# Kernel tuning notes

Hardware: AMD Instinct MI355X
Metric: run time of the kernel (lower is better)

The kernel has to match this reference:

```python
import jax, jax.numpy as jnp
import numpy as np

NUM_TOKENS = 32000
DIM = 1024
DEPTH = 4
HEADS = 16
DIM_HEAD = 64
FF_MULT = 4
DH_FF = int(DIM * FF_MULT * 2 / 3)  # 2730
B, N = 2, 2048
ROPE_THETA = 10000.0


def setup_inputs() -> dict:
    key = jax.random.key(0)
    ks = jax.random.split(key, 8)
    s = 0.02
    return {
        "tokens": jax.random.randint(ks[0], (B, N), 0, NUM_TOKENS),
        "token_emb": jax.random.normal(ks[1], (NUM_TOKENS, DIM)) * s,
        "attn_norm_w": jnp.ones((DEPTH, DIM)),
        "wqkv": jax.random.normal(ks[2], (DEPTH, DIM, 3 * HEADS * DIM_HEAD)) * s,
        "wo": jax.random.normal(ks[3], (DEPTH, HEADS * DIM_HEAD, DIM)) * s,
        "ff_norm_w": jnp.ones((DEPTH, DIM)),
        "ff_w1": jax.random.normal(ks[4], (DEPTH, DIM, 2 * DH_FF)) * s,
        "ff_b1": jnp.zeros((DEPTH, 2 * DH_FF)),
        "ff_w2": jax.random.normal(ks[5], (DEPTH, DH_FF, DIM)) * s,
        "ff_b2": jnp.zeros((DEPTH, DIM)),
        "final_norm_w": jnp.ones((DIM,)),
        "logits_w": jax.random.normal(ks[6], (DIM, NUM_TOKENS)) * s,
        "logits_b": jnp.zeros((NUM_TOKENS,)),
    }


def rmsnorm(x, w):
    eps = jnp.finfo(x.dtype).eps  # torch RMSNorm default eps
    var = jnp.mean(jnp.square(x), axis=-1, keepdims=True)
    return x * jax.lax.rsqrt(var + eps) * w


def rotate_half(x):
    x1, x2 = jnp.split(x, 2, axis=-1)
    return jnp.concatenate((-x2, x1), axis=-1)


def apply_rope(pos, t):
    return t * jnp.cos(pos) + rotate_half(t) * jnp.sin(pos)


def reference(tokens, token_emb, attn_norm_w, wqkv, wo, ff_norm_w,
              ff_w1, ff_b1, ff_w2, ff_b2, final_norm_w, logits_w, logits_b):
    b, n = tokens.shape
    x = token_emb[tokens]  # [b, n, dim]

    # rotary embedding table [n, dim_head]
    inv_freq = ROPE_THETA ** (-(jnp.arange(0, DIM_HEAD, 2, dtype=jnp.float32) / DIM_HEAD))
    freqs = jnp.arange(n, dtype=jnp.float32)[:, None] * inv_freq[None, :]
    pos = jnp.concatenate((freqs, freqs), axis=-1)

    scale = DIM_HEAD ** -0.5
    causal = jnp.triu(jnp.ones((n, n), dtype=bool), 1)

    for l in range(DEPTH):
        # --- attention ---
        h = rmsnorm(x, attn_norm_w[l])
        qkv = jnp.einsum('bnd,de->bne', h, wqkv[l])
        qkv = qkv.reshape(b, n, 3, HEADS, DIM_HEAD)
        qkv = jnp.transpose(qkv, (2, 0, 3, 1, 4))  # [3, b, h, n, d]
        q, k, v = qkv[0], qkv[1], qkv[2]
        q = apply_rope(pos, q)
        k = apply_rope(pos, k)
        q = q * scale
        sim = jnp.einsum('bhid,bhjd->bhij', q, k)
        sim = jnp.where(causal, -jnp.finfo(sim.dtype).max, sim)
        attn = jax.nn.softmax(sim, axis=-1)
        out = jnp.einsum('bhij,bhjd->bhid', attn, v)
        out = jnp.transpose(out, (0, 2, 1, 3)).reshape(b, n, HEADS * DIM_HEAD)
        x = jnp.einsum('bne,ed->bnd', out, wo[l]) + x

        # --- GEGLU feedforward ---
        h = rmsnorm(x, ff_norm_w[l])
        u = jnp.einsum('bnd,de->bne', h, ff_w1[l]) + ff_b1[l]
        u1, gate = jnp.split(u, 2, axis=-1)
        g = jax.nn.gelu(gate, approximate=False) * u1
        x = jnp.einsum('bne,ed->bnd', g, ff_w2[l]) + ff_b2[l] + x

    embed = rmsnorm(x, final_norm_w)
    logits = jnp.einsum('bnd,dv->bnv', embed, logits_w) + logits_b
    return logits
```

## Files before the change

kernel.cpp:

```cpp
#include <hip/hip_runtime.h>
#include <math.h>
#include <stdint.h>


using short8v = __attribute__((ext_vector_type(8))) short;
using f32x4   = __attribute__((ext_vector_type(4))) float;

__device__ __forceinline__ float b2f(short s) {
    union { unsigned u; float f; } v; v.u = ((unsigned)(unsigned short)s) << 16; return v.f;
}
__device__ __forceinline__ short f2b(float f) {
    union { float f; unsigned u; } v; v.f = f;
    unsigned r = v.u + 0x7FFFu + ((v.u >> 16) & 1u);
    return (short)(r >> 16);
}

__device__ __forceinline__ void mfma_n(f32x4& d, short8v a, short8v b) {
    asm("v_mfma_f32_16x16x32_bf16 %0, %1, %2, %0" : "+v"(d) : "v"(a), "v"(b));
}
__device__ __forceinline__ void mfma_f(f32x4& d, short8v a, short8v b) {
    asm("s_nop 1\n\tv_mfma_f32_16x16x32_bf16 %0, %1, %2, %0" : "+v"(d) : "v"(a), "v"(b));
}
#define MFMA_FENCE() do { __builtin_amdgcn_sched_barrier(0); \
    asm volatile("s_nop 7\n\ts_nop 7"); \
    __builtin_amdgcn_sched_barrier(0); } while (0)

__device__ __forceinline__ void gload16(const void* g, void* l) {
    __builtin_amdgcn_global_load_lds(
        (const __attribute__((address_space(1))) unsigned int*)(uintptr_t)g,
        (__attribute__((address_space(3))) unsigned int*)(uintptr_t)l,
        16, 0, 0);
}

#define BARX() do { asm volatile("" ::: "memory"); \
    __builtin_amdgcn_s_barrier(); asm volatile("" ::: "memory"); } while (0)
#define VMN(n) asm volatile("s_waitcnt vmcnt(" #n ")" ::: "memory")
#define LGKM0() do { asm volatile("s_waitcnt lgkmcnt(0)" ::: "memory"); \
    __builtin_amdgcn_sched_barrier(0); } while (0)

__global__ void rope_table_k(float* __restrict__ ct, float* __restrict__ st) {
    int i = blockIdx.x * 256 + threadIdx.x;
    int n = i >> 5, j = i & 31;
    float freq = expf(-(float)j * (9.210340371976184f / 32.f));
    float a = (float)n * freq;
    ct[i] = cosf(a);
    st[i] = sinf(a);
}

__global__ void embed_k(const int* __restrict__ tok, const float* __restrict__ emb,
                        float* __restrict__ x) {
    int row = blockIdx.x;
    int tk = tok[row];
    const float4* src = (const float4*)(emb + (size_t)tk * 1024);
    float4* dst = (float4*)(x + (size_t)row * 1024);
    dst[threadIdx.x] = src[threadIdx.x];
}

__global__ void wconv_k(const float* __restrict__ W, short* __restrict__ T,
                        int K, int N, int Kpad,
                        size_t w_lstride, size_t t_lstride) {
    W += blockIdx.z * w_lstride;
    T += blockIdx.z * t_lstride;
    int n0 = blockIdx.x * 32, k0 = blockIdx.y * 32;
    __shared__ float tile[32][33];
    int t = threadIdx.x;
    int kk = t >> 3, ns = (t & 7) * 4;
    float4 v = make_float4(0.f, 0.f, 0.f, 0.f);
    int gk = k0 + kk;
    if (gk < K) {
        if (n0 + ns + 3 < N) {
            v = *(const float4*)(W + (size_t)gk * N + n0 + ns);
        } else {
            float tmp[4] = {0.f, 0.f, 0.f, 0.f};
            #pragma unroll
            for (int j = 0; j < 4; ++j)
                if (n0 + ns + j < N) tmp[j] = W[(size_t)gk * N + n0 + ns + j];
            v = make_float4(tmp[0], tmp[1], tmp[2], tmp[3]);
        }
    }
    tile[kk][ns + 0] = v.x; tile[kk][ns + 1] = v.y;
    tile[kk][ns + 2] = v.z; tile[kk][ns + 3] = v.w;
    __syncthreads();
    int nn = t >> 3, ks = (t & 7) * 4;
    short o[4];
    #pragma unroll
    for (int j = 0; j < 4; ++j) o[j] = f2b(tile[ks + j][nn]);
    *(int2*)(T + (size_t)(n0 + nn) * Kpad + k0 + ks) = *(int2*)o;
}

__global__ void rmsnorm_k(const float* __restrict__ x, const float* __restrict__ wt,
                          short* __restrict__ out) {
    int row = blockIdx.x;
    int t = threadIdx.x;
    const float* xr = x + (size_t)row * 1024;
    float4 v = ((const float4*)xr)[t];
    float ss = v.x * v.x + v.y * v.y + v.z * v.z + v.w * v.w;
    #pragma unroll
    for (int off = 32; off > 0; off >>= 1) ss += __shfl_down(ss, off, 64);
    __shared__ float red[4];
    if ((t & 63) == 0) red[t >> 6] = ss;
    __syncthreads();
    float tot = red[0] + red[1] + red[2] + red[3];
    float inv = rsqrtf(tot * (1.f / 1024.f) + 1.1920929e-7f);
    float4 wv = ((const float4*)wt)[t];
    int2 pk;
    pk.x = (int)(unsigned short)f2b(v.x * inv * wv.x) |
           ((int)(unsigned short)f2b(v.y * inv * wv.y) << 16);
    pk.y = (int)(unsigned short)f2b(v.z * inv * wv.z) |
           ((int)(unsigned short)f2b(v.w * inv * wv.w) << 16);
    *(int2*)(out + (size_t)row * 1024 + t * 4) = pk;
}

__global__ void vt_k(const short* __restrict__ qkv, short* __restrict__ vt) {
    int id = blockIdx.x * 256 + threadIdx.x;
    int dt = id & 7, nt = (id >> 3) & 255, bh = id >> 11;
    int b = bh >> 4, h = bh & 15;
    short s[8][8];
    #pragma unroll
    for (int r = 0; r < 8; ++r)
        *(int4*)s[r] = *(const int4*)(qkv + (size_t)(b * 2048 + nt * 8 + r) * 3072
                                      + 2048 + h * 64 + dt * 8);
    #pragma unroll
    for (int cc = 0; cc < 8; ++cc) {
        short o4[8];
        #pragma unroll
        for (int r = 0; r < 8; ++r) o4[r] = s[r][cc];
        *(int4*)(vt + (size_t)(bh * 64 + dt * 8 + cc) * 2048 + nt * 8) = *(int4*)o4;
    }
}

__global__ void geglu_k(const short* __restrict__ u, short* __restrict__ gbuf) {
    int r = blockIdx.x;
    int c = blockIdx.y * 256 + threadIdx.x;
    if (c >= 2752) return;
    float v = 0.f;
    if (c < 2730) {
        float u1 = b2f(u[(size_t)r * 5460 + c]);
        float gt = b2f(u[(size_t)r * 5460 + 2730 + c]);
        v = 0.5f * gt * (1.f + erff(gt * 0.7071067811865475f)) * u1;
    }
    gbuf[(size_t)r * 2752 + c] = f2b(v);
}

template <bool BIAS, bool RES, bool OUTBF16>
__global__ __launch_bounds__(256, 2) void gemm2(
    const short* __restrict__ A, const short* __restrict__ Bt,
    const float* __restrict__ bias, const float* __restrict__ res,
    void* __restrict__ outp, int N, int lda, int ldb, int ksteps) {
    __shared__ __align__(16) short As[128 * 32];
    __shared__ __align__(16) short Bs[128 * 32];
    const int t = threadIdx.x;
    const int lane = t & 63;
    const int w = t >> 6, wm = w >> 1, wn = w & 1;
    const int c = lane & 15, g = lane >> 4;

    const int nwg = (int)gridDim.x;
    const int cpx = nwg >> 3;
    const int wg = ((int)blockIdx.x & 7) * cpx + ((int)blockIdx.x >> 3);
    const int m0 = (wg & 31) << 7;
    const int n0 = (wg >> 5) << 7;

    const int srow = w * 32 + (lane >> 2);
    const int sseg = (lane & 3) * 8;
    const short* ga0 = A  + (size_t)(m0 + srow) * lda + sseg;
    const short* ga1 = A  + (size_t)(m0 + srow + 16) * lda + sseg;
    const short* gb0 = Bt + (size_t)(n0 + srow) * ldb + sseg;
    const short* gb1 = Bt + (size_t)(n0 + srow + 16) * ldb + sseg;
    short* la0 = &As[(w * 2 + 0) * 512];
    short* la1 = &As[(w * 2 + 1) * 512];
    short* lb0 = &Bs[(w * 2 + 0) * 512];
    short* lb1 = &Bs[(w * 2 + 1) * 512];

    f32x4 acc[4][4] = {};

    for (int kt = 0; kt < ksteps; ++kt) {
        const int k0 = kt << 5;
        __syncthreads();
        gload16(ga0 + k0, la0);
        gload16(ga1 + k0, la1);
        gload16(gb0 + k0, lb0);
        gload16(gb1 + k0, lb1);
        __syncthreads();
        short8v af[4], bf[4];
        #pragma unroll
        for (int mi = 0; mi < 4; ++mi)
            af[mi] = *(const short8v*)&As[(wm * 64 + mi * 16 + c) * 32 + g * 8];
        #pragma unroll
        for (int ni = 0; ni < 4; ++ni)
            bf[ni] = *(const short8v*)&Bs[(wn * 64 + ni * 16 + c) * 32 + g * 8];
        #pragma unroll
        for (int mi = 0; mi < 4; ++mi)
            #pragma unroll
            for (int ni = 0; ni < 4; ++ni)
                mfma_n(acc[mi][ni], af[mi], bf[ni]);
    }
    MFMA_FENCE();
    #pragma unroll
    for (int mi = 0; mi < 4; ++mi) {
        #pragma unroll
        for (int ni = 0; ni < 4; ++ni) {
            int col = n0 + wn * 64 + ni * 16 + c;
            if (col < N) {
                float bv = BIAS ? bias[col] : 0.f;
                #pragma unroll
                for (int i = 0; i < 4; ++i) {
                    int row = m0 + wm * 64 + mi * 16 + g * 4 + i;
                    size_t off = (size_t)row * N + col;
                    float v = acc[mi][ni][i] + bv;
                    if (RES) v += res[off];
                    if (OUTBF16) ((short*)outp)[off] = f2b(v);
                    else         ((float*)outp)[off] = v;
                }
            }
        }
    }
}

template <bool BIAS, bool RES, bool OUTBF16, bool ROPE>
__global__ __launch_bounds__(512, 1) void gemm3(
    const short* __restrict__ A, const short* __restrict__ Bt,
    const float* __restrict__ bias, const float* __restrict__ res,
    void* __restrict__ outp, int N, int lda, int ldb, int nrowsB, int KT,
    const float* __restrict__ ct, const float* __restrict__ st) {
    __shared__ __align__(16) short L[49152];
    const int t = threadIdx.x;
    const int lane = t & 63;
    const int w = t >> 6;
    const int wm = w >> 2, wn = w & 3;
    const int c = lane & 15, g = lane >> 4;

    const int nwg = (int)gridDim.x, cpx = nwg >> 3;
    const int wg = ((int)blockIdx.x & 7) * cpx + ((int)blockIdx.x >> 3);
    const int m0 = (wg & 31) << 7;
    const int n0 = (wg >> 5) << 8;

    const int rS = t >> 3, sS = t & 7;
    const int sSw = (sS ^ (rS & 7)) << 3;
    size_t aoffh[2], broff[2][2];
    #pragma unroll
    for (int h = 0; h < 2; ++h)
        aoffh[h] = (size_t)(m0 + h * 64 + rS) * lda + sSw;
    #pragma unroll
    for (int h = 0; h < 2; ++h)
        #pragma unroll
        for (int i = 0; i < 2; ++i) {
            int brow = n0 + h * 128 + rS + i * 64;
            if (brow > nrowsB - 1) brow = nrowsB - 1;
            broff[h][i] = (size_t)brow * ldb + sSw;
        }
    short* ldsA[2][2];
    short* ldsB[2][2];
    #pragma unroll
    for (int p = 0; p < 2; ++p)
        #pragma unroll
        for (int h = 0; h < 2; ++h) {
            ldsA[p][h] = &L[(p * 2 + h) * 4096 + w * 512];
            ldsB[p][h] = &L[16384 + (p * 2 + h) * 8192 + w * 512];
        }

    const int cb0 = ((g * 8) ^ ((c & 7) * 8));
    const int vbA0 = wm * 4096 + c * 64 + cb0;
    const int vbA1 = vbA0 ^ 32;
    const int vbB0 = 16384 + (wn >> 1) * 8192 + (wn & 1) * 4096 + c * 64 + cb0;
    const int vbB1 = vbB0 ^ 32;

    #define STA3(p, h, kt) gload16(A + aoffh[h] + (kt) * 64, ldsA[p][h])
    #define STB3(p, h, kt) do { \
        gload16(Bt + broff[h][0] + (kt) * 64, ldsB[p][h]); \
        gload16(Bt + broff[h][1] + (kt) * 64, ldsB[p][h] + 4096); } while (0)
    #define LDA3(p, mi, ks) (*(const short8v*)&L[(p) * 8192 + (mi) * 1024 + ((ks) ? vbA1 : vbA0)])
    #define LDB3(p, ni, ks) (*(const short8v*)&L[(p) * 16384 + (ni) * 1024 + ((ks) ? vbB1 : vbB0)])
    #define MFMA8(MLO, NLO, BV) do { \
        _Pragma("unroll") for (int ks_ = 0; ks_ < 2; ++ks_) \
        _Pragma("unroll") for (int mi_ = 0; mi_ < 2; ++mi_) \
        _Pragma("unroll") for (int ni_ = 0; ni_ < 2; ++ni_) \
            mfma_n(acc[(MLO) + mi_][(NLO) + ni_], av[(MLO) + mi_][ks_], BV[(NLO) + ni_][ks_]); \
        } while (0)

    f32x4 acc[4][4] = {};
    short8v av[4][2], bc[4][2], bn[4][2];

    STB3(0, 1, 0); STB3(0, 0, 0); STA3(0, 0, 0); STA3(0, 1, 0);
    STB3(1, 1, 1); STB3(1, 0, 1); STA3(1, 0, 1); STA3(1, 1, 1);
    VMN(6);
    BARX();
    #pragma unroll
    for (int ni = 0; ni < 4; ++ni)
        #pragma unroll
        for (int ks = 0; ks < 2; ++ks)
            bc[ni][ks] = LDB3(0, ni, ks);
    LGKM0();
    BARX();
    asm volatile("s_nop 7\n\ts_nop 7");

    for (int KB = 0; KB < KT; KB += 2) {
        const bool st1 = (KB + 2 < KT);
        const bool st2 = (KB + 3 < KT);
        #pragma unroll
        for (int mi = 0; mi < 2; ++mi)
            #pragma unroll
            for (int ks = 0; ks < 2; ++ks) av[mi][ks] = LDA3(0, mi, ks);
        if (st1) STB3(0, 1, KB + 2);
        BARX();
        __builtin_amdgcn_s_setprio(1); MFMA8(0, 0, bc); __builtin_amdgcn_s_setprio(0);
        BARX();
        #pragma unroll
        for (int mi = 2; mi < 4; ++mi)
            #pragma unroll
            for (int ks = 0; ks < 2; ++ks) av[mi][ks] = LDA3(0, mi, ks);
        if (st1) { STB3(0, 0, KB + 2); VMN(6); } else { VMN(2); }
        BARX();
        __builtin_amdgcn_s_setprio(1); MFMA8(2, 0, bc); __builtin_amdgcn_s_setprio(0);
        BARX();
        #pragma unroll
        for (int ni = 0; ni < 2; ++ni)
            #pragma unroll
            for (int ks = 0; ks < 2; ++ks) bn[ni][ks] = LDB3(1, ni, ks);
        if (st1) STA3(0, 0, KB + 2);
        BARX();
        __builtin_amdgcn_s_setprio(1); MFMA8(0, 2, bc); __builtin_amdgcn_s_setprio(0);
        BARX();
        #pragma unroll
        for (int ni = 2; ni < 4; ++ni)
            #pragma unroll
            for (int ks = 0; ks < 2; ++ks) bn[ni][ks] = LDB3(1, ni, ks);
        if (st1) { STA3(0, 1, KB + 2); VMN(6); } else { VMN(0); }
        BARX();
        __builtin_amdgcn_s_setprio(1); MFMA8(2, 2, bc); __builtin_amdgcn_s_setprio(0);
        BARX();
        #pragma unroll
        for (int mi = 0; mi < 2; ++mi)
            #pragma unroll
            for (int ks = 0; ks < 2; ++ks) av[mi][ks] = LDA3(1, mi, ks);
        if (st2) STB3(1, 1, KB + 3);
        BARX();
        __builtin_amdgcn_s_setprio(1); MFMA8(0, 0, bn); __builtin_amdgcn_s_setprio(0);
        BARX();
        #pragma unroll
        for (int mi = 2; mi < 4; ++mi)
            #pragma unroll
            for (int ks = 0; ks < 2; ++ks) av[mi][ks] = LDA3(1, mi, ks);
        if (st2) STB3(1, 0, KB + 3);
        if (st1) VMN(6);
        BARX();
        __builtin_amdgcn_s_setprio(1); MFMA8(2, 0, bn); __builtin_amdgcn_s_setprio(0);
        BARX();
        if (st1) {
            #pragma unroll
            for (int ni = 0; ni < 2; ++ni)
                #pragma unroll
                for (int ks = 0; ks < 2; ++ks) bc[ni][ks] = LDB3(0, ni, ks);
        }
        if (st2) STA3(1, 0, KB + 3);
        BARX();
        __builtin_amdgcn_s_setprio(1); MFMA8(0, 2, bn); __builtin_amdgcn_s_setprio(0);
        BARX();
        if (st1) {
            #pragma unroll
            for (int ni = 2; ni < 4; ++ni)
                #pragma unroll
                for (int ks = 0; ks < 2; ++ks) bc[ni][ks] = LDB3(0, ni, ks);
        }
        if (st2) STA3(1, 1, KB + 3);
        if (st1) VMN(6);
        BARX();
        __builtin_amdgcn_s_setprio(1); MFMA8(2, 2, bn); __builtin_amdgcn_s_setprio(0);
        BARX();
    }

    MFMA_FENCE();

    if (ROPE) {
        const int colbase = n0 + wn * 64;
        const int sec = colbase >> 10;
        if (sec < 2) {
            const float sc = (sec == 0) ? 0.125f : 1.0f;
            #pragma unroll
            for (int mi = 0; mi < 4; ++mi)
                #pragma unroll
                for (int ni = 0; ni < 2; ++ni) {
                    const int col = colbase + ni * 16 + c;
                    const int jj = ni * 16 + c;
                    #pragma unroll
                    for (int i = 0; i < 4; ++i) {
                        int row = m0 + wm * 64 + mi * 16 + g * 4 + i;
                        int n = row & 2047;
                        float cv = ct[n * 32 + jj], sv = st[n * 32 + jj];
                        float a = acc[mi][ni][i], b = acc[mi][ni + 2][i];
                        ((short*)outp)[(size_t)row * N + col]      = f2b((a * cv - b * sv) * sc);
                        ((short*)outp)[(size_t)row * N + col + 32] = f2b((b * cv + a * sv) * sc);
                    }
                }
        } else {
            #pragma unroll
            for (int mi = 0; mi < 4; ++mi)
                #pragma unroll
                for (int ni = 0; ni < 4; ++ni) {
                    int col = colbase + ni * 16 + c;
                    #pragma unroll
                    for (int i = 0; i < 4; ++i) {
                        int row = m0 + wm * 64 + mi * 16 + g * 4 + i;
                        ((short*)outp)[(size_t)row * N + col] = f2b(acc[mi][ni][i]);
                    }
                }
        }
        return;
    }

    #pragma unroll
    for (int mi = 0; mi < 4; ++mi) {
        #pragma unroll
        for (int ni = 0; ni < 4; ++ni) {
            int col = n0 + wn * 64 + ni * 16 + c;
            if (col < N) {
                float bv = BIAS ? bias[col] : 0.f;
                #pragma unroll
                for (int i = 0; i < 4; ++i) {
                    int row = m0 + wm * 64 + mi * 16 + g * 4 + i;
                    size_t off = (size_t)row * N + col;
                    float v = acc[mi][ni][i] + bv;
                    if (RES) v += res[off];
                    if (OUTBF16) ((short*)outp)[off] = f2b(v);
                    else         ((float*)outp)[off] = v;
                }
            }
        }
    }
    #undef STA3
    #undef STB3
    #undef LDA3
    #undef LDB3
    #undef MFMA8
}

template <bool BIAS, bool RES, bool OUTBF16>
__global__ __launch_bounds__(512, 2) void gemm4(
    const short* __restrict__ A, const short* __restrict__ Bt,
    const float* __restrict__ bias, const float* __restrict__ res,
    void* __restrict__ outp, int N, int lda, int ldb, int nrowsB, int KT) {
    __shared__ __align__(16) short L[65536];
    const int t = threadIdx.x;
    const int lane = t & 63;
    const int w = t >> 6;
    const int wm = w >> 2, wn = w & 3;
    const int c = lane & 15, g = lane >> 4;

    const int nwg = (int)gridDim.x, cpx = nwg >> 3;
    const int wg = ((int)blockIdx.x & 7) * cpx + ((int)blockIdx.x >> 3);
    const int m0 = (wg & 15) << 8;
    const int n0 = (wg >> 4) << 8;

    const int sub0 = t & 63;
    const int seg0 = sub0 >> 4, r0 = sub0 & 15;
    const int slab0 = t >> 6, slab1 = slab0 + 8;
    const size_t aoff0 = (size_t)(m0 + slab0 * 16 + r0) * lda + seg0 * 8;
    const size_t aoff1 = (size_t)(m0 + slab1 * 16 + r0) * lda + seg0 * 8;
    int br0 = n0 + slab0 * 16 + r0; if (br0 > nrowsB - 1) br0 = nrowsB - 1;
    int br1 = n0 + slab1 * 16 + r0; if (br1 > nrowsB - 1) br1 = nrowsB - 1;
    const size_t boff0 = (size_t)br0 * ldb + seg0 * 8;
    const size_t boff1 = (size_t)br1 * ldb + seg0 * 8;

    char* Lb = (char*)L;
    const int rb = g * 256 + c * 16;

    #define STA4(p, kh, kt) do { \
        gload16(A + aoff0 + (kt) * 64 + (kh) * 32, Lb + ((p)*2+(kh))*16384 + w*1024); \
        gload16(A + aoff1 + (kt) * 64 + (kh) * 32, Lb + ((p)*2+(kh))*16384 + 8192 + w*1024); } while (0)
    #define STB4(p, kh, kt) do { \
        gload16(Bt + boff0 + (kt) * 64 + (kh) * 32, Lb + 65536 + ((p)*2+(kh))*16384 + w*1024); \
        gload16(Bt + boff1 + (kt) * 64 + (kh) * 32, Lb + 65536 + ((p)*2+(kh))*16384 + 8192 + w*1024); } while (0)
    #define LDA4(p, ks, mi) (*(const short8v*)(Lb + ((p)*2+(ks))*16384 + (wm*8+(mi))*1024 + rb))
    #define LDB4(p, ks, ni) (*(const short8v*)(Lb + 65536 + ((p)*2+(ks))*16384 + (wn*4+(ni))*1024 + rb))
    #define MFMAQ(MB) do { \
        _Pragma("unroll") for (int mi_ = 0; mi_ < 4; ++mi_) \
        _Pragma("unroll") for (int ni_ = 0; ni_ < 4; ++ni_) \
            mfma_n(acc[(MB) + mi_][ni_], av[mi_], bv[ni_]); } while (0)

    f32x4 acc[8][4] = {};
    short8v av[4], bv[4];

    STA4(0, 0, 0); STB4(0, 0, 0); STA4(0, 1, 0); STB4(0, 1, 0);
    VMN(4);
    BARX();
    asm volatile("s_nop 7\n\ts_nop 7");

    #define TILE4(p, pn, tc, stg2) do { \
        _Pragma("unroll") for (int mi = 0; mi < 4; ++mi) av[mi] = LDA4(p, 0, mi); \
        _Pragma("unroll") for (int ni = 0; ni < 4; ++ni) bv[ni] = LDB4(p, 0, ni); \
        if (stg2) STA4(pn, 0, (tc) + 1); \
        BARX(); \
        __builtin_amdgcn_s_setprio(1); MFMAQ(0); __builtin_amdgcn_s_setprio(0); \
        BARX(); \
        _Pragma("unroll") for (int mi = 0; mi < 4; ++mi) av[mi] = LDA4(p, 0, mi + 4); \
        if (stg2) { STB4(pn, 0, (tc) + 1); VMN(4); } else { VMN(0); } \
        BARX(); \
        __builtin_amdgcn_s_setprio(1); MFMAQ(4); __builtin_amdgcn_s_setprio(0); \
        BARX(); \
        _Pragma("unroll") for (int mi = 0; mi < 4; ++mi) av[mi] = LDA4(p, 1, mi); \
        _Pragma("unroll") for (int ni = 0; ni < 4; ++ni) bv[ni] = LDB4(p, 1, ni); \
        if (stg2) STA4(pn, 1, (tc) + 1); \
        BARX(); \
        __builtin_amdgcn_s_setprio(1); MFMAQ(0); __builtin_amdgcn_s_setprio(0); \
        BARX(); \
        _Pragma("unroll") for (int mi = 0; mi < 4; ++mi) av[mi] = LDA4(p, 1, mi + 4); \
        if (stg2) { STB4(pn, 1, (tc) + 1); VMN(4); } \
        BARX(); \
        __builtin_amdgcn_s_setprio(1); MFMAQ(4); __builtin_amdgcn_s_setprio(0); \
        BARX(); \
    } while (0)

    for (int kt = 0; kt < KT; kt += 2) {
        TILE4(0, 1, kt, true);
        TILE4(1, 0, kt + 1, (kt + 2 < KT));
    }
    #undef TILE4

    MFMA_FENCE();
    #pragma unroll
    for (int mi = 0; mi < 8; ++mi) {
        #pragma unroll
        for (int ni = 0; ni < 4; ++ni) {
            int col = n0 + wn * 64 + ni * 16 + c;
            if (col < N) {
                float bvv = BIAS ? bias[col] : 0.f;
                #pragma unroll
                for (int i = 0; i < 4; ++i) {
                    int row = m0 + wm * 128 + mi * 16 + g * 4 + i;
                    size_t off = (size_t)row * N + col;
                    float v = acc[mi][ni][i] + bvv;
                    if (RES) v += res[off];
                    if (OUTBF16) ((short*)outp)[off] = f2b(v);
                    else         ((float*)outp)[off] = v;
                }
            }
        }
    }
    #undef STA4
    #undef STB4
    #undef LDA4
    #undef LDB4
    #undef MFMAQ
}

__global__ __launch_bounds__(256, 2) void attn_fwd(
    const short* __restrict__ qkv, const short* __restrict__ vt,
    short* __restrict__ o) {
    const int qt = blockIdx.x, bh = blockIdx.y;
    const int b = bh >> 4, h = bh & 15;
    const int t = threadIdx.x, lane = t & 63, w = t >> 6;
    const int c = lane & 15, g = lane >> 4;
    __shared__ __align__(16) short Ks[128 * 72];
    __shared__ __align__(16) short Vs[64 * 136];
    __shared__ __align__(16) short Ps[128 * 136];

    #pragma unroll
    for (int i = 0; i < 4; ++i) {
        int idx = t + i * 256, r = idx >> 3, seg = idx & 7;
        *(int4*)&Ps[r * 136 + seg * 8] =
            *(const int4*)(qkv + (size_t)(b * 2048 + qt * 128 + r) * 3072 + h * 64 + seg * 8);
    }
    __syncthreads();
    short8v qf[2][2];
    #pragma unroll
    for (int mi = 0; mi < 2; ++mi)
        #pragma unroll
        for (int kk = 0; kk < 2; ++kk)
            qf[mi][kk] = *(const short8v*)&Ps[(w * 32 + mi * 16 + c) * 136 + kk * 32 + g * 8];

    f32x4 oacc[2][4] = {};
    float mrow[2][4], lrow[2][4];
    #pragma unroll
    for (int mi = 0; mi < 2; ++mi)
        #pragma unroll
        for (int i = 0; i < 4; ++i) { mrow[mi][i] = -3.0e38f; lrow[mi][i] = 0.f; }

    for (int jt = 0; jt <= qt; ++jt) {
        __syncthreads();
        #pragma unroll
        for (int i = 0; i < 4; ++i) {
            int idx = t + i * 256, r = idx >> 3, seg = idx & 7;
            *(int4*)&Ks[r * 72 + seg * 8] =
                *(const int4*)(qkv + (size_t)(b * 2048 + jt * 128 + r) * 3072
                               + 1024 + h * 64 + seg * 8);
        }
        #pragma unroll
        for (int i = 0; i < 4; ++i) {
            int idx = t + i * 256, d = idx >> 4, seg = idx & 15;
            *(int4*)&Vs[d * 136 + seg * 8] =
                *(const int4*)(vt + (size_t)(bh * 64 + d) * 2048 + jt * 128 + seg * 8);
        }
        __syncthreads();
        f32x4 sacc[2][8] = {};
        #pragma unroll
        for (int kk = 0; kk < 2; ++kk) {
            short8v kf[8];
            #pragma unroll
            for (int ni = 0; ni < 8; ++ni)
                kf[ni] = *(const short8v*)&Ks[(ni * 16 + c) * 72 + kk * 32 + g * 8];
            #pragma unroll
            for (int mi = 0; mi < 2; ++mi)
                #pragma unroll
                for (int ni = 0; ni < 8; ++ni) {
                    if (kk == 0) mfma_f(sacc[mi][ni], qf[mi][kk], kf[ni]);
                    else         mfma_n(sacc[mi][ni], qf[mi][kk], kf[ni]);
                }
        }
        MFMA_FENCE();
        if (jt == qt) {
            #pragma unroll
            for (int mi = 0; mi < 2; ++mi)
                #pragma unroll
                for (int ni = 0; ni < 8; ++ni)
                    #pragma unroll
                    for (int i = 0; i < 4; ++i) {
                        int qrow = w * 32 + mi * 16 + g * 4 + i;
                        int kcol = ni * 16 + c;
                        if (kcol > qrow) sacc[mi][ni][i] = -3.0e38f;
                    }
        }
        #pragma unroll
        for (int mi = 0; mi < 2; ++mi) {
            #pragma unroll
            for (int i = 0; i < 4; ++i) {
                float mx = sacc[mi][0][i];
                #pragma unroll
                for (int ni = 1; ni < 8; ++ni) mx = fmaxf(mx, sacc[mi][ni][i]);
                #pragma unroll
                for (int off = 1; off < 16; off <<= 1) mx = fmaxf(mx, __shfl_xor(mx, off, 64));
                float mnew = fmaxf(mrow[mi][i], mx);
                float alpha = __expf(mrow[mi][i] - mnew);
                mrow[mi][i] = mnew;
                float ls = 0.f;
                #pragma unroll
                for (int ni = 0; ni < 8; ++ni) {
                    float p = __expf(sacc[mi][ni][i] - mnew);
                    sacc[mi][ni][i] = p;
                    ls += p;
                }
                #pragma unroll
                for (int off = 1; off < 16; off <<= 1) ls += __shfl_xor(ls, off, 64);
                lrow[mi][i] = lrow[mi][i] * alpha + ls;
                #pragma unroll
                for (int df = 0; df < 4; ++df) oacc[mi][df][i] *= alpha;
            }
        }
        #pragma unroll
        for (int mi = 0; mi < 2; ++mi)
            #pragma unroll
            for (int ni = 0; ni < 8; ++ni)
                #pragma unroll
                for (int i = 0; i < 4; ++i)
                    Ps[(w * 32 + mi * 16 + g * 4 + i) * 136 + ni * 16 + c] =
                        f2b(sacc[mi][ni][i]);
        #pragma unroll
        for (int kk = 0; kk < 4; ++kk) {
            short8v pf[2], vf[4];
            #pragma unroll
            for (int mi = 0; mi < 2; ++mi)
                pf[mi] = *(const short8v*)&Ps[(w * 32 + mi * 16 + c) * 136 + kk * 32 + g * 8];
            #pragma unroll
            for (int df = 0; df < 4; ++df)
                vf[df] = *(const short8v*)&Vs[(df * 16 + c) * 136 + kk * 32 + g * 8];
            #pragma unroll
            for (int mi = 0; mi < 2; ++mi)
                #pragma unroll
                for (int df = 0; df < 4; ++df) {
                    if (kk == 0) mfma_f(oacc[mi][df], pf[mi], vf[df]);
                    else         mfma_n(oacc[mi][df], pf[mi], vf[df]);
                }
        }
    }
    MFMA_FENCE();
    #pragma unroll
    for (int mi = 0; mi < 2; ++mi)
        #pragma unroll
        for (int df = 0; df < 4; ++df)
            #pragma unroll
            for (int i = 0; i < 4; ++i) {
                int qrow = qt * 128 + w * 32 + mi * 16 + g * 4 + i;
                float v = oacc[mi][df][i] / lrow[mi][i];
                o[(size_t)(b * 2048 + qrow) * 1024 + h * 64 + df * 16 + c] = f2b(v);
            }
}

extern "C" void kernel_launch(void* const* d_in, const int* in_sizes, int n_in,
                              void* d_out, int out_size, void* d_ws, size_t ws_size,
                              hipStream_t stream) {
    (void)in_sizes; (void)n_in; (void)out_size; (void)ws_size;
    const int*   tokens = (const int*)d_in[0];
    const float* temb   = (const float*)d_in[1];
    const float* anw    = (const float*)d_in[2];
    const float* wqkv   = (const float*)d_in[3];
    const float* wo     = (const float*)d_in[4];
    const float* fnw    = (const float*)d_in[5];
    const float* fw1    = (const float*)d_in[6];
    const float* fb1    = (const float*)d_in[7];
    const float* fw2    = (const float*)d_in[8];
    const float* fb2    = (const float*)d_in[9];
    const float* finw   = (const float*)d_in[10];
    const float* lw     = (const float*)d_in[11];
    const float* lb     = (const float*)d_in[12];

    char* ws = (char*)d_ws;
    float* x    = (float*)(ws + 0);
    short* hb   = (short*)(ws + 16777216);
    short* qkv  = (short*)(ws + 25165824);
    short* ao   = (short*)(ws + 50331648);
    short* ub   = (short*)(ws + 58720256);
    short* gb   = (short*)(ws + 103448576);
    short* vtb  = (short*)(ws + 125992960);
    float* ct   = (float*)(ws + 134381568);
    float* st   = (float*)(ws + 134643712);
    short* qkvT = (short*)(ws + 134905856);
    short* woT  = (short*)(ws + 160071680);
    short* fw1T = (short*)(ws + 168460288);
    short* fw2T = (short*)(ws + 213549056);
    short* logT = (short*)(ws + 236093440);

    rope_table_k<<<256, 256, 0, stream>>>(ct, st);
    embed_k<<<4096, 256, 0, stream>>>(tokens, temb, x);

    wconv_k<<<dim3(96, 32, 4), 256, 0, stream>>>(
        wqkv, qkvT, 1024, 3072, 1024, (size_t)1024 * 3072, (size_t)3072 * 1024);
    wconv_k<<<dim3(32, 32, 4), 256, 0, stream>>>(
        wo, woT, 1024, 1024, 1024, (size_t)1024 * 1024, (size_t)1024 * 1024);
    wconv_k<<<dim3(172, 32, 4), 256, 0, stream>>>(
        fw1, fw1T, 1024, 5460, 1024, (size_t)1024 * 5460, (size_t)5504 * 1024);
    wconv_k<<<dim3(32, 86, 4), 256, 0, stream>>>(
        fw2, fw2T, 2730, 1024, 2752, (size_t)2730 * 1024, (size_t)1024 * 2752);
    wconv_k<<<dim3(1000, 32, 1), 256, 0, stream>>>(
        lw, logT, 1024, 32000, 1024, 0, 0);

    for (int l = 0; l < 4; ++l) {
        rmsnorm_k<<<4096, 256, 0, stream>>>(x, anw + l * 1024, hb);
        gemm3<false, false, true, true><<<32 * 12, 512, 0, stream>>>(
            hb, qkvT + (size_t)l * 3072 * 1024, nullptr, nullptr, qkv,
            3072, 1024, 1024, 3072, 16, ct, st);
        vt_k<<<256, 256, 0, stream>>>(qkv, vtb);
        attn_fwd<<<dim3(16, 32), 256, 0, stream>>>(qkv, vtb, ao);
        gemm2<false, true, false><<<32 * 8, 256, 0, stream>>>(
            ao, woT + (size_t)l * 1024 * 1024, nullptr, x, x, 1024, 1024, 1024, 32);
        rmsnorm_k<<<4096, 256, 0, stream>>>(x, fnw + l * 1024, hb);
        gemm3<true, false, true, false><<<32 * 22, 512, 0, stream>>>(
            hb, fw1T + (size_t)l * 5504 * 1024, fb1 + l * 5460, nullptr, ub,
            5460, 1024, 1024, 5504, 16, nullptr, nullptr);
        geglu_k<<<dim3(4096, 11), 256, 0, stream>>>(ub, gb);
        gemm2<true, true, false><<<32 * 8, 256, 0, stream>>>(
            gb, fw2T + (size_t)l * 1024 * 2752, fb2 + l * 1024, x, x, 1024, 2752, 2752, 86);
    }
    rmsnorm_k<<<4096, 256, 0, stream>>>(x, finw, hb);
    gemm4<true, false, false><<<2000, 512, 0, stream>>>(
        hb, logT, lb, nullptr, d_out, 32000, 1024, 1024, 32000, 16);
}
```

Measured before the change: 2.017 ms.

## Prefetch K/V into registers, reverse tile order, compute softmax row sums via MFMA

Attention blocks are now processed in reverse query-tile order, so the longest causal tiles are scheduled first and the tail is better balanced. The next K/V tile is loaded into registers while the current tile computes, hiding global-load latency behind MFMA work. The softmax row sum comes from an extra column of ones appended to V, computed as a fifth MFMA column, which removes the shuffle-reduction for l. This costs more registers and shared memory, and one extra MFMA per k-step, and it sums the bf16-rounded probabilities.

```diff
diff --git a/kernel.cpp b/kernel.cpp
--- a/kernel.cpp
+++ b/kernel.cpp
@@ -545,12 +545,13 @@
 __global__ __launch_bounds__(256, 2) void attn_fwd(
     const short* __restrict__ qkv, const short* __restrict__ vt,
     short* __restrict__ o) {
-    const int qt = blockIdx.x, bh = blockIdx.y;
+    const int qt = (int)gridDim.x - 1 - (int)blockIdx.x;
+    const int bh = blockIdx.y;
     const int b = bh >> 4, h = bh & 15;
     const int t = threadIdx.x, lane = t & 63, w = t >> 6;
     const int c = lane & 15, g = lane >> 4;
     __shared__ __align__(16) short Ks[128 * 72];
-    __shared__ __align__(16) short Vs[64 * 136];
+    __shared__ __align__(16) short Vs[80 * 136];
     __shared__ __align__(16) short Ps[128 * 136];
 
     #pragma unroll
@@ -559,6 +560,9 @@
         *(int4*)&Ps[r * 136 + seg * 8] =
             *(const int4*)(qkv + (size_t)(b * 2048 + qt * 128 + r) * 3072 + h * 64 + seg * 8);
     }
+    if (t < 136)
+        #pragma unroll
+        for (int r = 0; r < 16; ++r) Vs[(64 + r) * 136 + t] = 0x3F80;
     __syncthreads();
     short8v qf[2][2];
     #pragma unroll
@@ -567,29 +571,41 @@
         for (int kk = 0; kk < 2; ++kk)
             qf[mi][kk] = *(const short8v*)&Ps[(w * 32 + mi * 16 + c) * 136 + kk * 32 + g * 8];
 
-    f32x4 oacc[2][4] = {};
-    float mrow[2][4], lrow[2][4];
+    f32x4 oacc[2][5] = {};
+    float mrow[2][4];
     #pragma unroll
     for (int mi = 0; mi < 2; ++mi)
         #pragma unroll
-        for (int i = 0; i < 4; ++i) { mrow[mi][i] = -3.0e38f; lrow[mi][i] = 0.f; }
+        for (int i = 0; i < 4; ++i) mrow[mi][i] = -3.0e38f;
+
+    int4 kr[4], vr[4];
+    #define LOADKV(JT) do { \
+        _Pragma("unroll") for (int i = 0; i < 4; ++i) { \
+            int idx = t + i * 256, r = idx >> 3, seg = idx & 7; \
+            kr[i] = *(const int4*)(qkv + (size_t)(b * 2048 + (JT) * 128 + r) * 3072 \
+                                   + 1024 + h * 64 + seg * 8); } \
+        _Pragma("unroll") for (int i = 0; i < 4; ++i) { \
+            int idx = t + i * 256, d = idx >> 4, seg = idx & 15; \
+            vr[i] = *(const int4*)(vt + (size_t)(bh * 64 + d) * 2048 + (JT) * 128 + seg * 8); } \
+        } while (0)
+
+    LOADKV(0);
 
     for (int jt = 0; jt <= qt; ++jt) {
         __syncthreads();
         #pragma unroll
         for (int i = 0; i < 4; ++i) {
             int idx = t + i * 256, r = idx >> 3, seg = idx & 7;
-            *(int4*)&Ks[r * 72 + seg * 8] =
-                *(const int4*)(qkv + (size_t)(b * 2048 + jt * 128 + r) * 3072
-                               + 1024 + h * 64 + seg * 8);
+            *(int4*)&Ks[r * 72 + seg * 8] = kr[i];
         }
         #pragma unroll
         for (int i = 0; i < 4; ++i) {
             int idx = t + i * 256, d = idx >> 4, seg = idx & 15;
-            *(int4*)&Vs[d * 136 + seg * 8] =
-                *(const int4*)(vt + (size_t)(bh * 64 + d) * 2048 + jt * 128 + seg * 8);
+            *(int4*)&Vs[d * 136 + seg * 8] = vr[i];
         }
         __syncthreads();
+        if (jt < qt) LOADKV(jt + 1);
+
         f32x4 sacc[2][8] = {};
         #pragma unroll
         for (int kk = 0; kk < 2; ++kk) {
@@ -630,18 +646,11 @@
                 float mnew = fmaxf(mrow[mi][i], mx);
                 float alpha = __expf(mrow[mi][i] - mnew);
                 mrow[mi][i] = mnew;
-                float ls = 0.f;
-                #pragma unroll
-                for (int ni = 0; ni < 8; ++ni) {
-                    float p = __expf(sacc[mi][ni][i] - mnew);
-                    sacc[mi][ni][i] = p;
-                    ls += p;
-                }
-                #pragma unroll
-                for (int off = 1; off < 16; off <<= 1) ls += __shfl_xor(ls, off, 64);
-                lrow[mi][i] = lrow[mi][i] * alpha + ls;
-                #pragma unroll
-                for (int df = 0; df < 4; ++df) oacc[mi][df][i] *= alpha;
+                #pragma unroll
+                for (int ni = 0; ni < 8; ++ni)
+                    sacc[mi][ni][i] = __expf(sacc[mi][ni][i] - mnew);
+                #pragma unroll
+                for (int df = 0; df < 5; ++df) oacc[mi][df][i] *= alpha;
             }
         }
         #pragma unroll
@@ -654,22 +663,23 @@
                         f2b(sacc[mi][ni][i]);
         #pragma unroll
         for (int kk = 0; kk < 4; ++kk) {
-            short8v pf[2], vf[4];
+            short8v pf[2], vf[5];
             #pragma unroll
             for (int mi = 0; mi < 2; ++mi)
                 pf[mi] = *(const short8v*)&Ps[(w * 32 + mi * 16 + c) * 136 + kk * 32 + g * 8];
             #pragma unroll
-            for (int df = 0; df < 4; ++df)
+            for (int df = 0; df < 5; ++df)
                 vf[df] = *(const short8v*)&Vs[(df * 16 + c) * 136 + kk * 32 + g * 8];
             #pragma unroll
             for (int mi = 0; mi < 2; ++mi)
                 #pragma unroll
-                for (int df = 0; df < 4; ++df) {
+                for (int df = 0; df < 5; ++df) {
                     if (kk == 0) mfma_f(oacc[mi][df], pf[mi], vf[df]);
                     else         mfma_n(oacc[mi][df], pf[mi], vf[df]);
                 }
         }
     }
+    #undef LOADKV
     MFMA_FENCE();
     #pragma unroll
     for (int mi = 0; mi < 2; ++mi)
@@ -678,7 +688,7 @@
             #pragma unroll
             for (int i = 0; i < 4; ++i) {
                 int qrow = qt * 128 + w * 32 + mi * 16 + g * 4 + i;
-                float v = oacc[mi][df][i] / lrow[mi][i];
+                float v = oacc[mi][df][i] / oacc[mi][4][i];
                 o[(size_t)(b * 2048 + qrow) * 1024 + h * 64 + df * 16 + c] = f2b(v);
             }
 }
```

After: 2.074 ms. +2.8%, slower.

## Fuse V transpose into QKV GEMM epilogue and halve M-tile of N=1024 GEMMs

Applied to the files above, without the earlier changes.

The QKV GEMM epilogue now writes the V section directly in transposed [b,h,d,n] layout, which removes the separate vt_k kernel and its extra read and write of V. The gemm2 kernel used for the output projection and FF2 is changed to 64x128 tiles with 512 workgroups and launch bounds raised for higher occupancy, so the small N=1024 GEMMs fill more CUs. The transposed stores are 8-byte strided writes, and the smaller tiles give up some data reuse per workgroup.

```diff
diff --git a/kernel.cpp b/kernel.cpp
--- a/kernel.cpp
+++ b/kernel.cpp
@@ -111,24 +111,6 @@
     *(int2*)(out + (size_t)row * 1024 + t * 4) = pk;
 }
 
-__global__ void vt_k(const short* __restrict__ qkv, short* __restrict__ vt) {
-    int id = blockIdx.x * 256 + threadIdx.x;
-    int dt = id & 7, nt = (id >> 3) & 255, bh = id >> 11;
-    int b = bh >> 4, h = bh & 15;
-    short s[8][8];
-    #pragma unroll
-    for (int r = 0; r < 8; ++r)
-        *(int4*)s[r] = *(const int4*)(qkv + (size_t)(b * 2048 + nt * 8 + r) * 3072
-                                      + 2048 + h * 64 + dt * 8);
-    #pragma unroll
-    for (int cc = 0; cc < 8; ++cc) {
-        short o4[8];
-        #pragma unroll
-        for (int r = 0; r < 8; ++r) o4[r] = s[r][cc];
-        *(int4*)(vt + (size_t)(bh * 64 + dt * 8 + cc) * 2048 + nt * 8) = *(int4*)o4;
-    }
-}
-
 __global__ void geglu_k(const short* __restrict__ u, short* __restrict__ gbuf) {
     int r = blockIdx.x;
     int c = blockIdx.y * 256 + threadIdx.x;
@@ -143,11 +125,11 @@
 }
 
 template <bool BIAS, bool RES, bool OUTBF16>
-__global__ __launch_bounds__(256, 2) void gemm2(
+__global__ __launch_bounds__(256, 4) void gemm2h(
     const short* __restrict__ A, const short* __restrict__ Bt,
     const float* __restrict__ bias, const float* __restrict__ res,
     void* __restrict__ outp, int N, int lda, int ldb, int ksteps) {
-    __shared__ __align__(16) short As[128 * 32];
+    __shared__ __align__(16) short As[64 * 32];
     __shared__ __align__(16) short Bs[128 * 32];
     const int t = threadIdx.x;
     const int lane = t & 63;
@@ -157,46 +139,43 @@
     const int nwg = (int)gridDim.x;
     const int cpx = nwg >> 3;
     const int wg = ((int)blockIdx.x & 7) * cpx + ((int)blockIdx.x >> 3);
-    const int m0 = (wg & 31) << 7;
-    const int n0 = (wg >> 5) << 7;
-
-    const int srow = w * 32 + (lane >> 2);
+    const int m0 = (wg & 63) << 6;
+    const int n0 = (wg >> 6) << 7;
+
+    const int srow = w * 16 + (lane >> 2);
     const int sseg = (lane & 3) * 8;
     const short* ga0 = A  + (size_t)(m0 + srow) * lda + sseg;
-    const short* ga1 = A  + (size_t)(m0 + srow + 16) * lda + sseg;
-    const short* gb0 = Bt + (size_t)(n0 + srow) * ldb + sseg;
-    const short* gb1 = Bt + (size_t)(n0 + srow + 16) * ldb + sseg;
-    short* la0 = &As[(w * 2 + 0) * 512];
-    short* la1 = &As[(w * 2 + 1) * 512];
+    const short* gb0 = Bt + (size_t)(n0 + w * 32 + (lane >> 2)) * ldb + sseg;
+    const short* gb1 = Bt + (size_t)(n0 + w * 32 + 16 + (lane >> 2)) * ldb + sseg;
+    short* la0 = &As[w * 512];
     short* lb0 = &Bs[(w * 2 + 0) * 512];
     short* lb1 = &Bs[(w * 2 + 1) * 512];
 
-    f32x4 acc[4][4] = {};
+    f32x4 acc[2][4] = {};
 
     for (int kt = 0; kt < ksteps; ++kt) {
         const int k0 = kt << 5;
         __syncthreads();
         gload16(ga0 + k0, la0);
-        gload16(ga1 + k0, la1);
         gload16(gb0 + k0, lb0);
         gload16(gb1 + k0, lb1);
         __syncthreads();
-        short8v af[4], bf[4];
-        #pragma unroll
-        for (int mi = 0; mi < 4; ++mi)
-            af[mi] = *(const short8v*)&As[(wm * 64 + mi * 16 + c) * 32 + g * 8];
+        short8v af[2], bf[4];
+        #pragma unroll
+        for (int mi = 0; mi < 2; ++mi)
+            af[mi] = *(const short8v*)&As[(wm * 32 + mi * 16 + c) * 32 + g * 8];
         #pragma unroll
         for (int ni = 0; ni < 4; ++ni)
             bf[ni] = *(const short8v*)&Bs[(wn * 64 + ni * 16 + c) * 32 + g * 8];
         #pragma unroll
-        for (int mi = 0; mi < 4; ++mi)
+        for (int mi = 0; mi < 2; ++mi)
             #pragma unroll
             for (int ni = 0; ni < 4; ++ni)
                 mfma_n(acc[mi][ni], af[mi], bf[ni]);
     }
     MFMA_FENCE();
     #pragma unroll
-    for (int mi = 0; mi < 4; ++mi) {
+    for (int mi = 0; mi < 2; ++mi) {
         #pragma unroll
         for (int ni = 0; ni < 4; ++ni) {
             int col = n0 + wn * 64 + ni * 16 + c;
@@ -204,7 +183,7 @@
                 float bv = BIAS ? bias[col] : 0.f;
                 #pragma unroll
                 for (int i = 0; i < 4; ++i) {
-                    int row = m0 + wm * 64 + mi * 16 + g * 4 + i;
+                    int row = m0 + wm * 32 + mi * 16 + g * 4 + i;
                     size_t off = (size_t)row * N + col;
                     float v = acc[mi][ni][i] + bv;
                     if (RES) v += res[off];
@@ -221,7 +200,8 @@
     const short* __restrict__ A, const short* __restrict__ Bt,
     const float* __restrict__ bias, const float* __restrict__ res,
     void* __restrict__ outp, int N, int lda, int ldb, int nrowsB, int KT,
-    const float* __restrict__ ct, const float* __restrict__ st) {
+    const float* __restrict__ ct, const float* __restrict__ st,
+    short* __restrict__ vtb) {
     __shared__ __align__(16) short L[49152];
     const int t = threadIdx.x;
     const int lane = t & 63;
@@ -392,17 +372,21 @@
                     }
                 }
         } else {
-            #pragma unroll
-            for (int mi = 0; mi < 4; ++mi)
+            const int h64 = (colbase - 2048) >> 6;
+            #pragma unroll
+            for (int mi = 0; mi < 4; ++mi) {
+                const int r0 = m0 + wm * 64 + mi * 16 + g * 4;
+                const int bb = r0 >> 11, nn = r0 & 2047;
                 #pragma unroll
                 for (int ni = 0; ni < 4; ++ni) {
-                    int col = colbase + ni * 16 + c;
+                    const int d = ni * 16 + c;
+                    short s4[4];
                     #pragma unroll
-                    for (int i = 0; i < 4; ++i) {
-                        int row = m0 + wm * 64 + mi * 16 + g * 4 + i;
-                        ((short*)outp)[(size_t)row * N + col] = f2b(acc[mi][ni][i]);
-                    }
+                    for (int i = 0; i < 4; ++i) s4[i] = f2b(acc[mi][ni][i]);
+                    *(int2*)(vtb + (size_t)((bb * 16 + h64) * 64 + d) * 2048 + nn) =
+                        *(int2*)s4;
                 }
+            }
         }
         return;
     }
@@ -735,17 +719,16 @@
         rmsnorm_k<<<4096, 256, 0, stream>>>(x, anw + l * 1024, hb);
         gemm3<false, false, true, true><<<32 * 12, 512, 0, stream>>>(
             hb, qkvT + (size_t)l * 3072 * 1024, nullptr, nullptr, qkv,
-            3072, 1024, 1024, 3072, 16, ct, st);
-        vt_k<<<256, 256, 0, stream>>>(qkv, vtb);
+            3072, 1024, 1024, 3072, 16, ct, st, vtb);
         attn_fwd<<<dim3(16, 32), 256, 0, stream>>>(qkv, vtb, ao);
-        gemm2<false, true, false><<<32 * 8, 256, 0, stream>>>(
+        gemm2h<false, true, false><<<512, 256, 0, stream>>>(
             ao, woT + (size_t)l * 1024 * 1024, nullptr, x, x, 1024, 1024, 1024, 32);
         rmsnorm_k<<<4096, 256, 0, stream>>>(x, fnw + l * 1024, hb);
         gemm3<true, false, true, false><<<32 * 22, 512, 0, stream>>>(
             hb, fw1T + (size_t)l * 5504 * 1024, fb1 + l * 5460, nullptr, ub,
-            5460, 1024, 1024, 5504, 16, nullptr, nullptr);
+            5460, 1024, 1024, 5504, 16, nullptr, nullptr, nullptr);
         geglu_k<<<dim3(4096, 11), 256, 0, stream>>>(ub, gb);
-        gemm2<true, true, false><<<32 * 8, 256, 0, stream>>>(
+        gemm2h<true, true, false><<<512, 256, 0, stream>>>(
             gb, fw2T + (size_t)l * 1024 * 2752, fb2 + l * 1024, x, x, 1024, 2752, 2752, 86);
     }
     rmsnorm_k<<<4096, 256, 0, stream>>>(x, finw, hb);
```

Result: faster. 1.899 ms (-5.8%).
